# Performance work log

Measured on AMD Instinct MI355X. Metric: run time of the kernel, lower is better.

Reference implementation:

```python
import jax, jax.numpy as jnp
import numpy as np

POS = np.array([[0,3,0.5],[0,3,1.5],[0,3,2.5],[0,3,3.5],[0,3,4.5],[0,3,5.5],[1,0,0],[1,6,6],[2,0,6],[2,6,0],[3,0,0],[3,6,6],[4,0,6],[4,6,0],[5,0,0],[5,6,6],[6,0,6],[6,6,0],[7,0,0],[7,6,6],[8,0,6],[8,6,0],[9,0,0],[9,6,6],[10,0,6],[10,6,0],[11,0,0],[11,6,6],[12,0,6],[12,6,0],[13,0,0],[13,6,6],[14,0,6],[14,6,0],[15,0,0],[15,6,6],[16,0,6],[16,6,0],[17,0.5,0.5],[17,3,0.5],[17,5.5,0.5],[17,0.5,3],[17,3,3],[17,5.5,3],[17,0.5,5.5],[17,3,5.5],[17,5.5,5.5]], dtype=np.float32)  # (47,3) fixed buffer

B, S, D, H, FF, HID = 512, 47, 32, 4, 2048, 256

def _ln(x, w, b, eps=1e-5):
    mu = jnp.mean(x, -1, keepdims=True)
    var = jnp.mean((x - mu) ** 2, -1, keepdims=True)
    return (x - mu) * jax.lax.rsqrt(var + eps) * w + b

def _encoder_layer(h, wi, bi, wo, bo, l1w, l1b, f1w, f1b, f2w, f2b, l2w, l2b):
    # torch post-norm TransformerEncoderLayer; batch_first=False => attention over axis 0
    L, N, E = h.shape
    Dh = E // H
    qkv = h @ wi.T + bi                                  # (L,N,3E)
    q, k, v = jnp.split(qkv, 3, axis=-1)
    q = q.reshape(L, N, H, Dh); k = k.reshape(L, N, H, Dh); v = v.reshape(L, N, H, Dh)
    scores = jnp.einsum('lnhd,mnhd->nhlm', q, k) * (1.0 / np.sqrt(Dh))  # (N,H,L,L)
    a = jax.nn.softmax(scores, axis=-1)
    o = jnp.einsum('nhlm,mnhd->lnhd', a, v).reshape(L, N, E)
    h = _ln(h + (o @ wo.T + bo), l1w, l1b)
    ff = jax.nn.relu(h @ f1w.T + f1b) @ f2w.T + f2b
    return _ln(h + ff, l2w, l2b)

def setup_inputs():
    key = jax.random.key(0)
    ks = list(jax.random.split(key, 24))
    rn = lambda k, s, sc=0.05: jax.random.normal(k, s, jnp.float32) * sc
    return dict(
        x=jax.random.normal(ks[0], (B, S), jnp.float32),
        w_in=rn(ks[1], (D, 1)), b_in=rn(ks[2], (D,)),
        w_pos=rn(ks[3], (D, 3)), b_pos=rn(ks[4], (D,)),
        cls_token=rn(ks[5], (1, 1, D), 1.0),
        attn_in_w=rn(ks[6], (2, 3 * D, D)), attn_in_b=rn(ks[7], (2, 3 * D)),
        attn_out_w=rn(ks[8], (2, D, D)), attn_out_b=rn(ks[9], (2, D)),
        ln1_w=jnp.ones((2, D)), ln1_b=jnp.zeros((2, D)),
        ff1_w=rn(ks[10], (2, FF, D)), ff1_b=rn(ks[11], (2, FF)),
        ff2_w=rn(ks[12], (2, D, FF)), ff2_b=rn(ks[13], (2, D)),
        ln2_w=jnp.ones((2, D)), ln2_b=jnp.zeros((2, D)),
        out_w=rn(ks[14], (1, D)), out_b=rn(ks[15], (1,)),
        mlp_w0=rn(ks[16], (HID, S)), mlp_b0=rn(ks[17], (HID,)),
        mlp_w1=rn(ks[18], (HID, HID)), mlp_b1=rn(ks[19], (HID,)),
        mlp_w2=rn(ks[20], (1, HID)), mlp_b2=rn(ks[21], (1,)),
    )

def reference(x, w_in, b_in, w_pos, b_pos, cls_token, attn_in_w, attn_in_b, attn_out_w, attn_out_b, ln1_w, ln1_b, ff1_w, ff1_b, ff2_w, ff2_b, ln2_w, ln2_b, out_w, out_b, mlp_w0, mlp_b0, mlp_w1, mlp_b1, mlp_w2, mlp_b2):
    Bn = x.shape[0]
    h = x[..., None] * w_in[:, 0] + b_in                 # Linear(1,D): (B,S,D)
    h = h + (jnp.asarray(POS) @ w_pos.T + b_pos)         # pos projection (S,D)
    cls = jnp.broadcast_to(cls_token, (Bn, 1, D))
    h = jnp.concatenate([cls, h], axis=1)                # (B,S+1,D)
    for i in range(2):
        h = _encoder_layer(h, attn_in_w[i], attn_in_b[i], attn_out_w[i], attn_out_b[i], ln1_w[i], ln1_b[i], ff1_w[i], ff1_b[i], ff2_w[i], ff2_b[i], ln2_w[i], ln2_b[i])
    out = jax.nn.relu(h[:, 1:, :] @ out_w.T + out_b)[..., 0]   # (B,S); dropout = eval identity
    o = jax.nn.relu(out @ mlp_w0.T + mlp_b0)
    o = jax.nn.relu(o @ mlp_w1.T + mlp_b1)
    o = jax.nn.relu(o @ mlp_w2.T + mlp_b2)               # MLP ends with ReLU per source
    return o
```

## Files before the change

kernel.cpp:

```cpp
#include <hip/hip_runtime.h>

#define NB 512
#define NS 47
#define NP 48
#define DIM 32
#define NFF 2048
#define NHID 256
#define NROWS (NB * NP)
#define FTOK 96

#define VSTR 520
#define PSTR 72
#define USTR 136

typedef _Float16 f16x8 __attribute__((ext_vector_type(8)));
typedef _Float16 f16x4 __attribute__((ext_vector_type(4)));
typedef float f32x4 __attribute__((ext_vector_type(4)));

__constant__ float POSC[NS * 3] = {
  0,3,0.5f, 0,3,1.5f, 0,3,2.5f, 0,3,3.5f, 0,3,4.5f, 0,3,5.5f,
  1,0,0, 1,6,6, 2,0,6, 2,6,0, 3,0,0, 3,6,6, 4,0,6, 4,6,0,
  5,0,0, 5,6,6, 6,0,6, 6,6,0, 7,0,0, 7,6,6, 8,0,6, 8,6,0,
  9,0,0, 9,6,6, 10,0,6, 10,6,0, 11,0,0, 11,6,6, 12,0,6, 12,6,0,
  13,0,0, 13,6,6, 14,0,6, 14,6,0, 15,0,0, 15,6,6, 16,0,6, 16,6,0,
  17,0.5f,0.5f, 17,3,0.5f, 17,5.5f,0.5f, 17,0.5f,3, 17,3,3, 17,5.5f,3,
  17,0.5f,5.5f, 17,3,5.5f, 17,5.5f,5.5f
};

__global__ __launch_bounds__(256) void prep_embed_kernel(
    const float* __restrict__ w1, const float* __restrict__ w2,
    _Float16* __restrict__ w1h, _Float16* __restrict__ w2h,
    const float* __restrict__ x, const float* __restrict__ w_in,
    const float* __restrict__ b_in, const float* __restrict__ w_pos,
    const float* __restrict__ b_pos, const float* __restrict__ cls,
    float* __restrict__ h) {
  const int bx = blockIdx.x;
  if (bx < 512) {
    int idx = bx * 256 + threadIdx.x;
    w1h[idx] = (_Float16)w1[idx];
    int l = idx >> 16, r = idx & 65535, d = r >> 11, ff = r & 2047;
    int dst = ((l * 64 + (ff >> 5)) * 32 + d) * 32 + (ff & 31);
    w2h[dst] = (_Float16)w2[idx];
    return;
  }
  int idx = (bx - 512) * 256 + threadIdx.x;
  int r = idx >> 5, d = idx & 31;
  int l = r / NP, n = r - l * NP;
  float v;
  if (n == 0) {
    v = cls[d];
  } else {
    int s = n - 1;
    v = x[l * NS + s] * w_in[d] + b_in[d]
      + POSC[s * 3 + 0] * w_pos[d * 3 + 0]
      + POSC[s * 3 + 1] * w_pos[d * 3 + 1]
      + POSC[s * 3 + 2] * w_pos[d * 3 + 2] + b_pos[d];
  }
  h[idx] = v;
}

__global__ __launch_bounds__(256) void kv_kernel(
    const float* __restrict__ h, const float* __restrict__ wi, const float* __restrict__ bi,
    _Float16* __restrict__ Kp, _Float16* __restrict__ Vt) {
  __shared__ float ws_[512];
  __shared__ float bs_[16];
  const int t = threadIdx.x;
  const int nh = blockIdx.x >> 1;
  const int n = nh >> 2, hh = nh & 3;
  const int l = ((blockIdx.x & 1) << 8) | t;
  for (int i = t; i < 512; i += 256) {
    int sub = i >> 8, rem = i & 255;
    int jj = rem >> 5, d = rem & 31;
    ws_[i] = wi[((sub + 1) * 32 + hh * 8 + jj) * 32 + d];
  }
  if (t < 16) bs_[t] = bi[((t >> 3) + 1) * 32 + hh * 8 + (t & 7)];
  __syncthreads();
  const float4* hrow = (const float4*)(h + (l * NP + n) * 32);
  float4 hv[8];
  #pragma unroll
  for (int i = 0; i < 8; ++i) hv[i] = hrow[i];
  f16x8 kh, kl_, vh;
  #pragma unroll
  for (int jj = 0; jj < 8; ++jj) {
    float k0 = bs_[jj], k1 = 0.f, k2 = 0.f, k3 = 0.f;
    float v0 = bs_[8 + jj], v1 = 0.f, v2 = 0.f, v3 = 0.f;
    #pragma unroll
    for (int d4 = 0; d4 < 8; ++d4) {
      float4 hvv = hv[d4];
      k0 += hvv.x * ws_[jj * 32 + 4 * d4 + 0];
      k1 += hvv.y * ws_[jj * 32 + 4 * d4 + 1];
      k2 += hvv.z * ws_[jj * 32 + 4 * d4 + 2];
      k3 += hvv.w * ws_[jj * 32 + 4 * d4 + 3];
      v0 += hvv.x * ws_[256 + jj * 32 + 4 * d4 + 0];
      v1 += hvv.y * ws_[256 + jj * 32 + 4 * d4 + 1];
      v2 += hvv.z * ws_[256 + jj * 32 + 4 * d4 + 2];
      v3 += hvv.w * ws_[256 + jj * 32 + 4 * d4 + 3];
    }
    float kv = (k0 + k1) + (k2 + k3);
    float vv = (v0 + v1) + (v2 + v3);
    kh[jj] = (_Float16)kv; kl_[jj] = (_Float16)(kv - (float)kh[jj]);
    vh[jj] = (_Float16)vv;
  }
  _Float16* kdst = Kp + ((size_t)nh * 512 + l) * 16;
  *(f16x8*)(kdst) = kh;
  *(f16x8*)(kdst + 8) = kl_;
  #pragma unroll
  for (int d = 0; d < 8; ++d) Vt[(size_t)nh * 4096 + d * 512 + l] = vh[d];
}

__global__ __launch_bounds__(256, 3) void attn_mfma_kernel(
    const float* __restrict__ h, const float* __restrict__ wi, const float* __restrict__ bi,
    const _Float16* __restrict__ Kp, const _Float16* __restrict__ Vt,
    float* __restrict__ o) {
  __shared__ alignas(16) _Float16 khi[512 * 8];
  __shared__ alignas(16) _Float16 klo[512 * 8];
  __shared__ alignas(16) _Float16 vts[8 * VSTR];
  __shared__ alignas(16) float hq_pls[4608];
  __shared__ alignas(16) _Float16 qf[128 * 16];
  __shared__ float wsq[256];
  __shared__ float bq[8];
  const int bx = blockIdx.x;
  const int nh = bx >> 2, qc = bx & 3;
  const int n = nh >> 2, hh = nh & 3;
  const int t = threadIdx.x;
  const int lane = t & 63, wv = t >> 6;
  const int c = lane & 15, g = lane >> 4;

  const _Float16* kg = Kp + (size_t)nh * 8192;
  for (int r = t; r < 512; r += 256) {
    const uint4* src = (const uint4*)(kg + r * 16);
    uint4 a = src[0], b = src[1];
    *(uint4*)(khi + r * 8) = a;
    *(uint4*)(klo + r * 8) = b;
  }
  {
    const _Float16* vg = Vt + (size_t)nh * 4096;
    for (int i = t; i < 512; i += 256) {
      int d = i >> 6, seg = i & 63;
      *(uint4*)(vts + d * VSTR + seg * 8) = *(const uint4*)(vg + d * 512 + seg * 8);
    }
  }
  wsq[t] = wi[(hh * 8 + (t & 7)) * 32 + (t >> 3)];
  if (t < 8) bq[t] = bi[hh * 8 + t];
  float* hq = hq_pls;

  #pragma unroll
  for (int rp = 0; rp < 2; ++rp) {
    {
      int row = t >> 2, quar = t & 3;
      const float4* src =
          (const float4*)(h + (((qc * 128 + rp * 64 + row) * NP) + n) * 32 + quar * 8);
      float4 a = src[0], b = src[1];
      __syncthreads();
      *(float4*)(hq + row * 36 + quar * 8) = a;
      *(float4*)(hq + row * 36 + quar * 8 + 4) = b;
    }
    __syncthreads();
    {
      int row = t >> 2, pr = t & 3;
      #pragma unroll
      for (int u = 0; u < 2; ++u) {
        int jj = pr * 2 + u;
        float a = bq[jj];
        #pragma unroll
        for (int d = 0; d < 32; ++d) a += hq[row * 36 + d] * wsq[d * 8 + jj];
        _Float16 qh = (_Float16)a;
        _Float16 ql = (_Float16)(a - (float)qh);
        qf[(rp * 64 + row) * 16 + jj] = qh;
        qf[(rp * 64 + row) * 16 + 8 + jj] = ql;
      }
    }
    __syncthreads();
  }

  const f16x8 hz = {(_Float16)0,(_Float16)0,(_Float16)0,(_Float16)0,
                    (_Float16)0,(_Float16)0,(_Float16)0,(_Float16)0};
  const f32x4 zf = {0.f, 0.f, 0.f, 0.f};
  _Float16* pls_ = (_Float16*)hq_pls;
  _Float16* mypA = pls_ + wv * (16 * PSTR);
  _Float16* mypB = pls_ + (4 + wv) * (16 * PSTR);
  const int q0A = qc * 128 + wv * 16;
  const int q0B = q0A + 64;

  f16x8 aqA = hz, aqB = hz;
  if (g < 3) {
    aqA = *(const f16x8*)(qf + (wv * 16 + c) * 16 + (g & 1) * 8);
    aqB = *(const f16x8*)(qf + (64 + wv * 16 + c) * 16 + (g & 1) * 8);
  }
  f32x4 accA = {0.f, 0.f, 0.f, 0.f}, accB = {0.f, 0.f, 0.f, 0.f};
  float lsA[4] = {0.f, 0.f, 0.f, 0.f}, lsB[4] = {0.f, 0.f, 0.f, 0.f};

  for (int ch = 0; ch < 8; ++ch) {
    const int kb = ch * 64;
    #pragma unroll
    for (int kt = 0; kt < 4; ++kt) {
      f16x8 bk = hz;
      if (g < 2)       bk = *(const f16x8*)(khi + (kb + kt * 16 + c) * 8);
      else if (g == 2) bk = *(const f16x8*)(klo + (kb + kt * 16 + c) * 8);
      f32x4 sA = __builtin_amdgcn_mfma_f32_16x16x32_f16(aqA, bk, zf, 0, 0, 0);
      f32x4 sB = __builtin_amdgcn_mfma_f32_16x16x32_f16(aqB, bk, zf, 0, 0, 0);
      #pragma unroll
      for (int r = 0; r < 4; ++r) {
        float pA = __expf(sA[r] * 0.35355339059327373f - 2.0f);
        float pB = __expf(sB[r] * 0.35355339059327373f - 2.0f);
        _Float16 phA = (_Float16)pA;
        _Float16 phB = (_Float16)pB;
        lsA[r] += (float)phA;
        lsB[r] += (float)phB;
        mypA[(g * 4 + r) * PSTR + kt * 16 + c] = phA;
        mypB[(g * 4 + r) * PSTR + kt * 16 + c] = phB;
      }
    }
    #pragma unroll
    for (int half = 0; half < 2; ++half) {
      f16x8 bv = hz;
      if (c < 8) bv = *(const f16x8*)(vts + c * VSTR + kb + half * 32 + g * 8);
      f16x8 apA = *(const f16x8*)(mypA + c * PSTR + half * 32 + g * 8);
      f16x8 apB = *(const f16x8*)(mypB + c * PSTR + half * 32 + g * 8);
      accA = __builtin_amdgcn_mfma_f32_16x16x32_f16(apA, bv, accA, 0, 0, 0);
      accB = __builtin_amdgcn_mfma_f32_16x16x32_f16(apB, bv, accB, 0, 0, 0);
    }
  }
  #pragma unroll
  for (int m = 1; m < 16; m <<= 1) {
    #pragma unroll
    for (int r = 0; r < 4; ++r) {
      lsA[r] += __shfl_xor(lsA[r], m, 64);
      lsB[r] += __shfl_xor(lsB[r], m, 64);
    }
  }
  if (c < 8) {
    #pragma unroll
    for (int r = 0; r < 4; ++r) {
      o[((q0A + g * 4 + r) * NP + n) * 32 + hh * 8 + c] = accA[r] / lsA[r];
      o[((q0B + g * 4 + r) * NP + n) * 32 + hh * 8 + c] = accB[r] / lsB[r];
    }
  }
}

__global__ __launch_bounds__(256) void proj_ln1_kernel(
    const float* __restrict__ o, const float* __restrict__ wo, const float* __restrict__ bo,
    const float* __restrict__ lw, const float* __restrict__ lb, float* __restrict__ h) {
  __shared__ float wos[32 * 33];
  __shared__ float pre[64 * 33];
  const int g = blockIdx.x, t = threadIdx.x;
  for (int i = t; i < 1024; i += 256) wos[(i >> 5) * 33 + (i & 31)] = wo[i];
  __syncthreads();
  const int subr = t >> 2, jq = t & 3;
  const int r = g * 64 + subr;
  const float4* orow = (const float4*)(o + r * 32);
  float4 ov[8];
  #pragma unroll
  for (int i = 0; i < 8; ++i) ov[i] = orow[i];
  const float* hres = h + r * 32 + jq * 8;
  #pragma unroll
  for (int jj = 0; jj < 8; ++jj) {
    int j = jq * 8 + jj;
    float a0 = bo[j], a1 = 0.f, a2 = 0.f, a3 = 0.f;
    #pragma unroll
    for (int d4 = 0; d4 < 8; ++d4) {
      float4 vv = ov[d4];
      a0 += vv.x * wos[j * 33 + 4 * d4 + 0];
      a1 += vv.y * wos[j * 33 + 4 * d4 + 1];
      a2 += vv.z * wos[j * 33 + 4 * d4 + 2];
      a3 += vv.w * wos[j * 33 + 4 * d4 + 3];
    }
    pre[subr * 33 + j] = (a0 + a1) + (a2 + a3) + hres[jj];
  }
  __syncthreads();
  if (t < 64) {
    float mu = 0.f;
    #pragma unroll
    for (int d = 0; d < 32; ++d) mu += pre[t * 33 + d];
    mu *= (1.f / 32.f);
    float var = 0.f;
    #pragma unroll
    for (int d = 0; d < 32; ++d) { float dv = pre[t * 33 + d] - mu; var += dv * dv; }
    float rs = rsqrtf(var * (1.f / 32.f) + 1e-5f);
    float* hrow = h + (g * 64 + t) * 32;
    #pragma unroll
    for (int d = 0; d < 32; ++d)
      hrow[d] = (pre[t * 33 + d] - mu) * rs * lw[d] + lb[d];
  }
}

__global__ __launch_bounds__(256, 1) void ff_fused_kernel(
    const float* __restrict__ h, const _Float16* __restrict__ w1h,
    const float* __restrict__ b1, const _Float16* __restrict__ w2h,
    const float* __restrict__ b2, const float* __restrict__ lw,
    const float* __restrict__ lb, const float* __restrict__ ow,
    const float* __restrict__ ob,
    const float* __restrict__ m0w, const float* __restrict__ m0b,
    const float* __restrict__ m1w, const float* __restrict__ m1b,
    const float* __restrict__ m2w, const float* __restrict__ m2b,
    float* __restrict__ out, int do_head) {
  __shared__ alignas(16) _Float16 ubuf[4][2][16 * USTR];
  __shared__ alignas(16) float yw[4][FTOK * 33];
  __shared__ float sv2[2][48];
  __shared__ float hid[NHID];
  __shared__ float red[4];
  const int t = threadIdx.x;
  const int lane = t & 63;
  const int wv = t >> 6;
  const int nl = lane & 15;
  const int g = lane >> 4;
  const int g4 = g * 4;
  const int r0 = blockIdx.x * FTOK;

  f16x8 hfrag[6];
  #pragma unroll
  for (int tt = 0; tt < 6; ++tt) {
    const float4 h0 = *(const float4*)(h + (r0 + tt * 16 + nl) * 32 + g * 8);
    const float4 h1 = *(const float4*)(h + (r0 + tt * 16 + nl) * 32 + g * 8 + 4);
    hfrag[tt][0] = (_Float16)h0.x; hfrag[tt][1] = (_Float16)h0.y;
    hfrag[tt][2] = (_Float16)h0.z; hfrag[tt][3] = (_Float16)h0.w;
    hfrag[tt][4] = (_Float16)h1.x; hfrag[tt][5] = (_Float16)h1.y;
    hfrag[tt][6] = (_Float16)h1.z; hfrag[tt][7] = (_Float16)h1.w;
  }

  f32x4 acc0[6], acc1[6];
  #pragma unroll
  for (int tt = 0; tt < 6; ++tt) {
    acc0[tt] = (f32x4){0.f, 0.f, 0.f, 0.f};
    acc1[tt] = (f32x4){0.f, 0.f, 0.f, 0.f};
  }
  const f32x4 zero = {0.f, 0.f, 0.f, 0.f};
  const int ffbase = wv * 512;

  #pragma unroll
  for (int sc = 0; sc < 4; ++sc) {
    const int ffb = ffbase + sc * 128;
    f16x8 wf[8];
    float4 bv[8];
    #pragma unroll
    for (int ft = 0; ft < 8; ++ft) {
      wf[ft] = *(const f16x8*)(w1h + (ffb + ft * 16 + nl) * 32 + g * 8);
      bv[ft] = *(const float4*)(b1 + ffb + ft * 16 + g4);
    }
    f16x8 w2f0[4], w2f1[4];
    #pragma unroll
    for (int kk = 0; kk < 4; ++kk) {
      const _Float16* cb = w2h + ((ffb >> 5) + kk) * 1024;
      w2f0[kk] = *(const f16x8*)(cb + nl * 32 + g * 8);
      w2f1[kk] = *(const f16x8*)(cb + (16 + nl) * 32 + g * 8);
    }
    #pragma unroll
    for (int tt = 0; tt < 6; ++tt) {
      _Float16* ub = ubuf[wv][tt & 1];
      f32x4 cc[8];
      #pragma unroll
      for (int ft = 0; ft < 8; ++ft)
        cc[ft] = __builtin_amdgcn_mfma_f32_16x16x32_f16(wf[ft], hfrag[tt], zero, 0, 0, 0);
      #pragma unroll
      for (int ft = 0; ft < 8; ++ft) {
        f16x4 uv;
        uv[0] = (_Float16)fmaxf(cc[ft][0] + bv[ft].x, 0.f);
        uv[1] = (_Float16)fmaxf(cc[ft][1] + bv[ft].y, 0.f);
        uv[2] = (_Float16)fmaxf(cc[ft][2] + bv[ft].z, 0.f);
        uv[3] = (_Float16)fmaxf(cc[ft][3] + bv[ft].w, 0.f);
        *(f16x4*)(ub + nl * USTR + ft * 16 + g4) = uv;
      }
      #pragma unroll
      for (int kk = 0; kk < 4; ++kk) {
        f16x8 uf = *(const f16x8*)(ub + nl * USTR + kk * 32 + g * 8);
        acc0[tt] = __builtin_amdgcn_mfma_f32_16x16x32_f16(uf, w2f0[kk], acc0[tt], 0, 0, 0);
        acc1[tt] = __builtin_amdgcn_mfma_f32_16x16x32_f16(uf, w2f1[kk], acc1[tt], 0, 0, 0);
      }
    }
  }
  #pragma unroll
  for (int tt = 0; tt < 6; ++tt) {
    #pragma unroll
    for (int r = 0; r < 4; ++r) {
      yw[wv][(tt * 16 + g4 + r) * 33 + nl]      = acc0[tt][r];
      yw[wv][(tt * 16 + g4 + r) * 33 + 16 + nl] = acc1[tt][r];
    }
  }
  __syncthreads();

  float* pre = (float*)ubuf;
  {
    int idx = t;
    #pragma unroll
    for (int u = 0; u < 12; ++u, idx += 256) {
      int tok = idx >> 5, d = idx & 31;
      int off = tok * 33 + d;
      float v = yw[0][off] + yw[1][off] + yw[2][off] + yw[3][off]
              + b2[d] + h[(r0 + tok) * 32 + d];
      pre[off] = v;
    }
  }
  __syncthreads();

  if (t < FTOK) {
    float mu = 0.f;
    #pragma unroll
    for (int d = 0; d < 32; ++d) mu += pre[t * 33 + d];
    mu *= (1.f / 32.f);
    float var = 0.f;
    #pragma unroll
    for (int d = 0; d < 32; ++d) { float dv = pre[t * 33 + d] - mu; var += dv * dv; }
    float rs = rsqrtf(var * (1.f / 32.f) + 1e-5f);
    const int rr = r0 + t;
    float* hrow = (float*)h + (size_t)rr * 32;
    float hn[32];
    #pragma unroll
    for (int d = 0; d < 32; ++d) {
      hn[d] = (pre[t * 33 + d] - mu) * rs * lw[d] + lb[d];
      hrow[d] = hn[d];
    }
    if (do_head) {
      int ll = t / 48, n = t - ll * 48;
      if (n > 0) {
        float a = ob[0];
        #pragma unroll
        for (int d = 0; d < 32; ++d) a += hn[d] * ow[d];
        sv2[ll][n - 1] = fmaxf(a, 0.f);
      }
    }
  }

  if (do_head) {
    __syncthreads();
    for (int ll = 0; ll < 2; ++ll) {
      const int l = (r0 / 48) + ll;
      {
        float a = m0b[t];
        const float* wr = m0w + t * NS;
        #pragma unroll
        for (int s = 0; s < NS; ++s) a += sv2[ll][s] * wr[s];
        hid[t] = fmaxf(a, 0.f);
      }
      __syncthreads();
      {
        float a = m1b[t];
        const float4* wr = (const float4*)(m1w + t * NHID);
        #pragma unroll 8
        for (int j4 = 0; j4 < 64; ++j4) {
          float4 w = wr[j4];
          a += hid[4 * j4 + 0] * w.x + hid[4 * j4 + 1] * w.y
             + hid[4 * j4 + 2] * w.z + hid[4 * j4 + 3] * w.w;
        }
        float h2 = fmaxf(a, 0.f);
        float part = h2 * m2w[t];
        #pragma unroll
        for (int off = 32; off > 0; off >>= 1) part += __shfl_down(part, off, 64);
        if ((t & 63) == 0) red[t >> 6] = part;
      }
      __syncthreads();
      if (t == 0) out[l] = fmaxf(red[0] + red[1] + red[2] + red[3] + m2b[0], 0.f);
      __syncthreads();
    }
  }
}

extern "C" void kernel_launch(void* const* d_in, const int* in_sizes, int n_in,
                              void* d_out, int out_size, void* d_ws, size_t ws_size,
                              hipStream_t stream) {
  (void)in_sizes; (void)n_in; (void)out_size; (void)ws_size;
  const float* x     = (const float*)d_in[0];
  const float* w_in  = (const float*)d_in[1];
  const float* b_in  = (const float*)d_in[2];
  const float* w_pos = (const float*)d_in[3];
  const float* b_pos = (const float*)d_in[4];
  const float* cls   = (const float*)d_in[5];
  const float* wi    = (const float*)d_in[6];
  const float* bi    = (const float*)d_in[7];
  const float* wo    = (const float*)d_in[8];
  const float* bo    = (const float*)d_in[9];
  const float* l1w   = (const float*)d_in[10];
  const float* l1b   = (const float*)d_in[11];
  const float* f1w   = (const float*)d_in[12];
  const float* f1b   = (const float*)d_in[13];
  const float* f2w   = (const float*)d_in[14];
  const float* f2b   = (const float*)d_in[15];
  const float* l2w   = (const float*)d_in[16];
  const float* l2b   = (const float*)d_in[17];
  const float* ow    = (const float*)d_in[18];
  const float* ob    = (const float*)d_in[19];
  const float* m0w   = (const float*)d_in[20];
  const float* m0b   = (const float*)d_in[21];
  const float* m1w   = (const float*)d_in[22];
  const float* m1b   = (const float*)d_in[23];
  const float* m2w   = (const float*)d_in[24];
  const float* m2b   = (const float*)d_in[25];
  float* out = (float*)d_out;

  float* ws   = (float*)d_ws;
  float* h    = ws;
  float* o    = ws + 786432;
  float* R2   = ws + 1572864;
  _Float16* Kp = (_Float16*)R2;
  _Float16* Vt = (_Float16*)(R2 + 786432);
  _Float16* w1h = (_Float16*)(ws + 2776576);
  _Float16* w2h = (_Float16*)(ws + 2842112);

  prep_embed_kernel<<<3584, 256, 0, stream>>>(f1w, f2w, w1h, w2h,
                                              x, w_in, b_in, w_pos, b_pos, cls, h);
  for (int L = 0; L < 2; ++L) {
    kv_kernel<<<384, 256, 0, stream>>>(h, wi + L * 3072, bi + L * 96, Kp, Vt);
    attn_mfma_kernel<<<768, 256, 0, stream>>>(h, wi + L * 3072, bi + L * 96, Kp, Vt, o);
    proj_ln1_kernel<<<384, 256, 0, stream>>>(o, wo + L * 1024, bo + L * 32,
                                             l1w + L * 32, l1b + L * 32, h);
    ff_fused_kernel<<<256, 256, 0, stream>>>(h, w1h + L * 65536, f1b + L * NFF,
                                             w2h + L * 65536, f2b + L * 32,
                                             l2w + L * 32, l2b + L * 32,
                                             ow, ob, m0w, m0b, m1w, m1b, m2w, m2b,
                                             out, L);
  }
}
```

Before: 151.9 us.

## Double-buffer FF weight registers with 64-wide chunks and single LDS buffer

Restructures the fused feed-forward loop into 64-wide hidden chunks whose W1, bias and W2 register fragments are loaded one chunk ahead (ping-pong A/B register sets), so global weight loads overlap the MFMA work of the previous chunk. The per-wave LDS staging buffer drops from double-buffered 128-wide to single 64-wide, and a separate pre_s buffer replaces the aliasing of ubuf for the layernorm stage. This trades extra live registers and smaller per-chunk MFMA batches for less load stall; the single ub buffer reused across tt iterations relies on in-wave ordering of LDS accesses.

```diff
diff --git a/kernel.cpp b/kernel.cpp
--- a/kernel.cpp
+++ b/kernel.cpp
@@ -11,7 +11,7 @@
 
 #define VSTR 520
 #define PSTR 72
-#define USTR 136
+#define USTR 72
 
 typedef _Float16 f16x8 __attribute__((ext_vector_type(8)));
 typedef _Float16 f16x4 __attribute__((ext_vector_type(4)));
@@ -294,8 +294,9 @@
     const float* __restrict__ m1w, const float* __restrict__ m1b,
     const float* __restrict__ m2w, const float* __restrict__ m2b,
     float* __restrict__ out, int do_head) {
-  __shared__ alignas(16) _Float16 ubuf[4][2][16 * USTR];
+  __shared__ alignas(16) _Float16 ubuf[4][16 * USTR];
   __shared__ alignas(16) float yw[4][FTOK * 33];
+  __shared__ alignas(16) float pre_s[FTOK * 33];
   __shared__ float sv2[2][48];
   __shared__ float hid[NHID];
   __shared__ float red[4];
@@ -326,48 +327,65 @@
   }
   const f32x4 zero = {0.f, 0.f, 0.f, 0.f};
   const int ffbase = wv * 512;
-
-  #pragma unroll
-  for (int sc = 0; sc < 4; ++sc) {
-    const int ffb = ffbase + sc * 128;
-    f16x8 wf[8];
-    float4 bv[8];
-    #pragma unroll
-    for (int ft = 0; ft < 8; ++ft) {
-      wf[ft] = *(const f16x8*)(w1h + (ffb + ft * 16 + nl) * 32 + g * 8);
-      bv[ft] = *(const float4*)(b1 + ffb + ft * 16 + g4);
-    }
-    f16x8 w2f0[4], w2f1[4];
-    #pragma unroll
-    for (int kk = 0; kk < 4; ++kk) {
-      const _Float16* cb = w2h + ((ffb >> 5) + kk) * 1024;
-      w2f0[kk] = *(const f16x8*)(cb + nl * 32 + g * 8);
-      w2f1[kk] = *(const f16x8*)(cb + (16 + nl) * 32 + g * 8);
-    }
-    #pragma unroll
-    for (int tt = 0; tt < 6; ++tt) {
-      _Float16* ub = ubuf[wv][tt & 1];
-      f32x4 cc[8];
-      #pragma unroll
-      for (int ft = 0; ft < 8; ++ft)
-        cc[ft] = __builtin_amdgcn_mfma_f32_16x16x32_f16(wf[ft], hfrag[tt], zero, 0, 0, 0);
-      #pragma unroll
-      for (int ft = 0; ft < 8; ++ft) {
-        f16x4 uv;
-        uv[0] = (_Float16)fmaxf(cc[ft][0] + bv[ft].x, 0.f);
-        uv[1] = (_Float16)fmaxf(cc[ft][1] + bv[ft].y, 0.f);
-        uv[2] = (_Float16)fmaxf(cc[ft][2] + bv[ft].z, 0.f);
-        uv[3] = (_Float16)fmaxf(cc[ft][3] + bv[ft].w, 0.f);
-        *(f16x4*)(ub + nl * USTR + ft * 16 + g4) = uv;
-      }
-      #pragma unroll
-      for (int kk = 0; kk < 4; ++kk) {
-        f16x8 uf = *(const f16x8*)(ub + nl * USTR + kk * 32 + g * 8);
-        acc0[tt] = __builtin_amdgcn_mfma_f32_16x16x32_f16(uf, w2f0[kk], acc0[tt], 0, 0, 0);
-        acc1[tt] = __builtin_amdgcn_mfma_f32_16x16x32_f16(uf, w2f1[kk], acc1[tt], 0, 0, 0);
-      }
-    }
-  }
+  _Float16* ub = ubuf[wv];
+
+  f16x8 wfA[4], wfB[4], w2A[4], w2B[4];
+  float4 bvA[4], bvB[4];
+
+#define LOADW(WF, W2, BV, SC) {                                            \
+    const int fb_ = ffbase + (SC) * 64;                                    \
+    _Pragma("unroll")                                                      \
+    for (int ft = 0; ft < 4; ++ft) {                                       \
+      WF[ft] = *(const f16x8*)(w1h + (fb_ + ft * 16 + nl) * 32 + g * 8);   \
+      BV[ft] = *(const float4*)(b1 + fb_ + ft * 16 + g4);                  \
+    }                                                                      \
+    _Pragma("unroll")                                                      \
+    for (int kk = 0; kk < 2; ++kk) {                                       \
+      const _Float16* cb_ = w2h + ((fb_ >> 5) + kk) * 1024;                \
+      W2[kk * 2 + 0] = *(const f16x8*)(cb_ + nl * 32 + g * 8);             \
+      W2[kk * 2 + 1] = *(const f16x8*)(cb_ + (16 + nl) * 32 + g * 8);      \
+    }                                                                      \
+  }
+
+#define COMPUTE(WF, W2, BV) {                                              \
+    _Pragma("unroll")                                                      \
+    for (int tt = 0; tt < 6; ++tt) {                                       \
+      f32x4 cc[4];                                                         \
+      _Pragma("unroll")                                                    \
+      for (int ft = 0; ft < 4; ++ft)                                       \
+        cc[ft] = __builtin_amdgcn_mfma_f32_16x16x32_f16(WF[ft], hfrag[tt], \
+                                                        zero, 0, 0, 0);    \
+      _Pragma("unroll")                                                    \
+      for (int ft = 0; ft < 4; ++ft) {                                     \
+        f16x4 uv;                                                          \
+        uv[0] = (_Float16)fmaxf(cc[ft][0] + BV[ft].x, 0.f);                \
+        uv[1] = (_Float16)fmaxf(cc[ft][1] + BV[ft].y, 0.f);                \
+        uv[2] = (_Float16)fmaxf(cc[ft][2] + BV[ft].z, 0.f);                \
+        uv[3] = (_Float16)fmaxf(cc[ft][3] + BV[ft].w, 0.f);                \
+        *(f16x4*)(ub + nl * USTR + ft * 16 + g4) = uv;                     \
+      }                                                                    \
+      _Pragma("unroll")                                                    \
+      for (int kk = 0; kk < 2; ++kk) {                                     \
+        f16x8 uf = *(const f16x8*)(ub + nl * USTR + kk * 32 + g * 8);      \
+        acc0[tt] = __builtin_amdgcn_mfma_f32_16x16x32_f16(                 \
+            uf, W2[kk * 2 + 0], acc0[tt], 0, 0, 0);                        \
+        acc1[tt] = __builtin_amdgcn_mfma_f32_16x16x32_f16(                 \
+            uf, W2[kk * 2 + 1], acc1[tt], 0, 0, 0);                        \
+      }                                                                    \
+    }                                                                      \
+  }
+
+  LOADW(wfA, w2A, bvA, 0)
+  #pragma unroll
+  for (int sc = 0; sc < 8; sc += 2) {
+    if (sc + 1 < 8) LOADW(wfB, w2B, bvB, sc + 1)
+    COMPUTE(wfA, w2A, bvA)
+    if (sc + 2 < 8) LOADW(wfA, w2A, bvA, sc + 2)
+    COMPUTE(wfB, w2B, bvB)
+  }
+#undef LOADW
+#undef COMPUTE
+
   #pragma unroll
   for (int tt = 0; tt < 6; ++tt) {
     #pragma unroll
@@ -378,7 +396,6 @@
   }
   __syncthreads();
 
-  float* pre = (float*)ubuf;
   {
     int idx = t;
     #pragma unroll
@@ -387,7 +404,7 @@
       int off = tok * 33 + d;
       float v = yw[0][off] + yw[1][off] + yw[2][off] + yw[3][off]
               + b2[d] + h[(r0 + tok) * 32 + d];
-      pre[off] = v;
+      pre_s[off] = v;
     }
   }
   __syncthreads();
@@ -395,18 +412,18 @@
   if (t < FTOK) {
     float mu = 0.f;
     #pragma unroll
-    for (int d = 0; d < 32; ++d) mu += pre[t * 33 + d];
+    for (int d = 0; d < 32; ++d) mu += pre_s[t * 33 + d];
     mu *= (1.f / 32.f);
     float var = 0.f;
     #pragma unroll
-    for (int d = 0; d < 32; ++d) { float dv = pre[t * 33 + d] - mu; var += dv * dv; }
+    for (int d = 0; d < 32; ++d) { float dv = pre_s[t * 33 + d] - mu; var += dv * dv; }
     float rs = rsqrtf(var * (1.f / 32.f) + 1e-5f);
     const int rr = r0 + t;
     float* hrow = (float*)h + (size_t)rr * 32;
     float hn[32];
     #pragma unroll
     for (int d = 0; d < 32; ++d) {
-      hn[d] = (pre[t * 33 + d] - mu) * rs * lw[d] + lb[d];
+      hn[d] = (pre_s[t * 33 + d] - mu) * rs * lw[d] + lb[d];
       hrow[d] = hn[d];
     }
     if (do_head) {
```

After: 151.4 us. Within noise of the previous version (-0.3%).

## Keep FF hidden activations in registers by chaining MFMA output layout into second GEMM

Applied to the files above, without the earlier changes.

The fused feed-forward kernel no longer stages the ReLU hidden tile through shared memory between the two GEMMs. The first MFMA's accumulator fragments are converted directly into the B operand of the second MFMA, with W2 fragments loaded in a matching permuted layout, and the output is written back transposed. This removes LDS writes and reads per token tile and frees the ubuf shared memory, at the cost of smaller FF chunks per iteration (32 instead of 128) and more global weight loads in a non-unrolled loop.

```diff
diff --git a/kernel.cpp b/kernel.cpp
--- a/kernel.cpp
+++ b/kernel.cpp
@@ -11,7 +11,6 @@
 
 #define VSTR 520
 #define PSTR 72
-#define USTR 136
 
 typedef _Float16 f16x8 __attribute__((ext_vector_type(8)));
 typedef _Float16 f16x4 __attribute__((ext_vector_type(4)));
@@ -294,8 +293,8 @@
     const float* __restrict__ m1w, const float* __restrict__ m1b,
     const float* __restrict__ m2w, const float* __restrict__ m2b,
     float* __restrict__ out, int do_head) {
-  __shared__ alignas(16) _Float16 ubuf[4][2][16 * USTR];
   __shared__ alignas(16) float yw[4][FTOK * 33];
+  __shared__ alignas(16) float pre_s[FTOK * 33];
   __shared__ float sv2[2][48];
   __shared__ float hid[NHID];
   __shared__ float red[4];
@@ -325,60 +324,51 @@
     acc1[tt] = (f32x4){0.f, 0.f, 0.f, 0.f};
   }
   const f32x4 zero = {0.f, 0.f, 0.f, 0.f};
-  const int ffbase = wv * 512;
-
-  #pragma unroll
-  for (int sc = 0; sc < 4; ++sc) {
-    const int ffb = ffbase + sc * 128;
-    f16x8 wf[8];
-    float4 bv[8];
-    #pragma unroll
-    for (int ft = 0; ft < 8; ++ft) {
-      wf[ft] = *(const f16x8*)(w1h + (ffb + ft * 16 + nl) * 32 + g * 8);
-      bv[ft] = *(const float4*)(b1 + ffb + ft * 16 + g4);
-    }
-    f16x8 w2f0[4], w2f1[4];
-    #pragma unroll
-    for (int kk = 0; kk < 4; ++kk) {
-      const _Float16* cb = w2h + ((ffb >> 5) + kk) * 1024;
-      w2f0[kk] = *(const f16x8*)(cb + nl * 32 + g * 8);
-      w2f1[kk] = *(const f16x8*)(cb + (16 + nl) * 32 + g * 8);
+
+  for (int sc = 0; sc < 16; ++sc) {
+    const int ffb = wv * 512 + sc * 32;
+    f16x8 wf0 = *(const f16x8*)(w1h + (ffb + nl) * 32 + g * 8);
+    f16x8 wf1 = *(const f16x8*)(w1h + (ffb + 16 + nl) * 32 + g * 8);
+    float4 bv0 = *(const float4*)(b1 + ffb + g4);
+    float4 bv1 = *(const float4*)(b1 + ffb + 16 + g4);
+    const _Float16* cb = w2h + (ffb >> 5) * 1024;
+    f16x4 a0lo = *(const f16x4*)(cb + nl * 32 + g4);
+    f16x4 a0hi = *(const f16x4*)(cb + nl * 32 + 16 + g4);
+    f16x4 a1lo = *(const f16x4*)(cb + (16 + nl) * 32 + g4);
+    f16x4 a1hi = *(const f16x4*)(cb + (16 + nl) * 32 + 16 + g4);
+    f16x8 A0, A1;
+    #pragma unroll
+    for (int j = 0; j < 4; ++j) {
+      A0[j] = a0lo[j]; A0[4 + j] = a0hi[j];
+      A1[j] = a1lo[j]; A1[4 + j] = a1hi[j];
     }
     #pragma unroll
     for (int tt = 0; tt < 6; ++tt) {
-      _Float16* ub = ubuf[wv][tt & 1];
-      f32x4 cc[8];
-      #pragma unroll
-      for (int ft = 0; ft < 8; ++ft)
-        cc[ft] = __builtin_amdgcn_mfma_f32_16x16x32_f16(wf[ft], hfrag[tt], zero, 0, 0, 0);
-      #pragma unroll
-      for (int ft = 0; ft < 8; ++ft) {
-        f16x4 uv;
-        uv[0] = (_Float16)fmaxf(cc[ft][0] + bv[ft].x, 0.f);
-        uv[1] = (_Float16)fmaxf(cc[ft][1] + bv[ft].y, 0.f);
-        uv[2] = (_Float16)fmaxf(cc[ft][2] + bv[ft].z, 0.f);
-        uv[3] = (_Float16)fmaxf(cc[ft][3] + bv[ft].w, 0.f);
-        *(f16x4*)(ub + nl * USTR + ft * 16 + g4) = uv;
-      }
-      #pragma unroll
-      for (int kk = 0; kk < 4; ++kk) {
-        f16x8 uf = *(const f16x8*)(ub + nl * USTR + kk * 32 + g * 8);
-        acc0[tt] = __builtin_amdgcn_mfma_f32_16x16x32_f16(uf, w2f0[kk], acc0[tt], 0, 0, 0);
-        acc1[tt] = __builtin_amdgcn_mfma_f32_16x16x32_f16(uf, w2f1[kk], acc1[tt], 0, 0, 0);
-      }
+      f32x4 cc0 = __builtin_amdgcn_mfma_f32_16x16x32_f16(wf0, hfrag[tt], zero, 0, 0, 0);
+      f32x4 cc1 = __builtin_amdgcn_mfma_f32_16x16x32_f16(wf1, hfrag[tt], zero, 0, 0, 0);
+      f16x8 uB;
+      uB[0] = (_Float16)fmaxf(cc0[0] + bv0.x, 0.f);
+      uB[1] = (_Float16)fmaxf(cc0[1] + bv0.y, 0.f);
+      uB[2] = (_Float16)fmaxf(cc0[2] + bv0.z, 0.f);
+      uB[3] = (_Float16)fmaxf(cc0[3] + bv0.w, 0.f);
+      uB[4] = (_Float16)fmaxf(cc1[0] + bv1.x, 0.f);
+      uB[5] = (_Float16)fmaxf(cc1[1] + bv1.y, 0.f);
+      uB[6] = (_Float16)fmaxf(cc1[2] + bv1.z, 0.f);
+      uB[7] = (_Float16)fmaxf(cc1[3] + bv1.w, 0.f);
+      acc0[tt] = __builtin_amdgcn_mfma_f32_16x16x32_f16(A0, uB, acc0[tt], 0, 0, 0);
+      acc1[tt] = __builtin_amdgcn_mfma_f32_16x16x32_f16(A1, uB, acc1[tt], 0, 0, 0);
     }
   }
   #pragma unroll
   for (int tt = 0; tt < 6; ++tt) {
     #pragma unroll
     for (int r = 0; r < 4; ++r) {
-      yw[wv][(tt * 16 + g4 + r) * 33 + nl]      = acc0[tt][r];
-      yw[wv][(tt * 16 + g4 + r) * 33 + 16 + nl] = acc1[tt][r];
+      yw[wv][(tt * 16 + nl) * 33 + g4 + r]      = acc0[tt][r];
+      yw[wv][(tt * 16 + nl) * 33 + 16 + g4 + r] = acc1[tt][r];
     }
   }
   __syncthreads();
 
-  float* pre = (float*)ubuf;
   {
     int idx = t;
     #pragma unroll
@@ -387,7 +377,7 @@
       int off = tok * 33 + d;
       float v = yw[0][off] + yw[1][off] + yw[2][off] + yw[3][off]
               + b2[d] + h[(r0 + tok) * 32 + d];
-      pre[off] = v;
+      pre_s[off] = v;
     }
   }
   __syncthreads();
@@ -395,18 +385,18 @@
   if (t < FTOK) {
     float mu = 0.f;
     #pragma unroll
-    for (int d = 0; d < 32; ++d) mu += pre[t * 33 + d];
+    for (int d = 0; d < 32; ++d) mu += pre_s[t * 33 + d];
     mu *= (1.f / 32.f);
     float var = 0.f;
     #pragma unroll
-    for (int d = 0; d < 32; ++d) { float dv = pre[t * 33 + d] - mu; var += dv * dv; }
+    for (int d = 0; d < 32; ++d) { float dv = pre_s[t * 33 + d] - mu; var += dv * dv; }
     float rs = rsqrtf(var * (1.f / 32.f) + 1e-5f);
     const int rr = r0 + t;
     float* hrow = (float*)h + (size_t)rr * 32;
     float hn[32];
     #pragma unroll
     for (int d = 0; d < 32; ++d) {
-      hn[d] = (pre[t * 33 + d] - mu) * rs * lw[d] + lb[d];
+      hn[d] = (pre_s[t * 33 + d] - mu) * rs * lw[d] + lb[d];
       hrow[d] = hn[d];
     }
     if (do_head) {
```

Measured after the change: 151.2 us. No clear change (-0.4%).
